# Optimization experiments

Measured on AMD Instinct MI355X. Metric: run time of the kernel, lower is better.

Reference implementation:

```python
import jax, jax.numpy as jnp
import numpy as np

TESS = 5  # number of cells
N_POINTS = 16_777_216


def _make_basis(nc):
    # Continuity constraints of piecewise-affine velocity v(x)=a_c x + b_c at
    # interior knots x_i = i/nc:  a_i x_i + b_i - a_{i+1} x_i - b_{i+1} = 0.
    L = np.zeros((nc - 1, 2 * nc), dtype=np.float64)
    for i in range(1, nc):
        xb = i / nc
        L[i - 1, 2 * (i - 1)] = xb
        L[i - 1, 2 * (i - 1) + 1] = 1.0
        L[i - 1, 2 * i] = -xb
        L[i - 1, 2 * i + 1] = -1.0
    _, _, Vt = np.linalg.svd(L)
    B = Vt[nc - 1:].T  # (2*nc, nc+1) orthonormal null-space basis ('svd')
    return B.astype(np.float32)


def setup_inputs() -> dict:
    key = jax.random.key(0)
    k1, k2 = jax.random.split(key)
    x = jax.random.uniform(k1, (N_POINTS,), dtype=jnp.float32)
    theta = jax.random.normal(k2, (1, TESS + 1), dtype=jnp.float32) * 0.5
    B = jnp.asarray(_make_basis(TESS))
    return {"x": x, "theta": theta, "B": B}


def reference(x, theta, B):
    EPS = 1e-7
    TINY = 1e-12
    BIG = 1e10
    nc = B.shape[0] // 2
    x = jnp.clip(x, EPS, 1.0 - EPS)
    A = (B @ theta[0]).reshape(nc, 2)  # per-cell affine velocity [a_c, b_c]
    a_all, b_all = A[:, 0], A[:, 1]
    c0 = jnp.clip(jnp.floor(x * nc), 0, nc - 1).astype(jnp.int32)

    def step(carry, _):
        xc, c, t, logder = carry
        a = a_all[c]
        b = b_all[c]
        v = a * xc + b
        big = jnp.abs(a) > 1e-8
        sa = jnp.where(big, a, 1.0)
        eat = jnp.exp(a * t)
        # exact in-cell ODE solution psi(x, t)
        psi = jnp.where(big, xc * eat + (b / sa) * (eat - 1.0), xc + b * t)
        right = v >= 0
        xb = jnp.where(right, (c + 1).astype(xc.dtype), c.astype(xc.dtype)) / nc
        den = xc + b / sa
        sden = jnp.where(jnp.abs(den) > TINY, den, TINY)
        ratio = (xb + b / sa) / sden
        thit_a = jnp.log(jnp.maximum(ratio, TINY)) / sa  # time to reach boundary
        sb = jnp.where(jnp.abs(b) > TINY, b, TINY)
        thit_b = (xb - xc) / sb
        thit = jnp.where(big, thit_a, thit_b)
        valid = (jnp.abs(v) > TINY) & (thit >= 0.0) & jnp.where(big, ratio > 0.0, True)
        thit = jnp.where(valid, thit, BIG)
        hits = thit < t
        dt = jnp.where(hits, thit, t)
        x_new = jnp.where(hits, xb, psi)
        c_new = jnp.where(hits, jnp.clip(c + jnp.where(right, 1, -1), 0, nc - 1), c)
        return (x_new, c_new, t - dt, logder + a * dt), None

    init = (x, c0, jnp.ones_like(x), jnp.zeros_like(x))
    (z, _, _, logder), _ = jax.lax.scan(step, init, None, length=nc + 2)
    # log(dz/dx) = sum_c a_c * dt_c  (derivative of flow is exp of integrated slope)
    return z, logder
```

## Files before the change

kernel.cpp:

```cpp
#include <hip/hip_runtime.h>

#define NC 5
#define VEC 8

typedef float fvec4 __attribute__((ext_vector_type(4)));

__global__ __launch_bounds__(256) void flow_cpab_kernel(
    const float* __restrict__ x, const float* __restrict__ theta,
    const float* __restrict__ B, float* __restrict__ out, int n)
{
    __shared__ float4 s_k0[NC];
    __shared__ float4 s_q[12];
    __shared__ float4 s_thr[12];
    __shared__ float4 s_pA[60];
    __shared__ float4 s_pB[60];

    const int tid = threadIdx.x;
    const float EPS  = 1e-7f;
    const float TINY = 1e-12f;
    const float BIG  = 1e10f;
    const float LOG_TINY = -27.631021115928547f;

    const int base = (blockIdx.x * blockDim.x + tid) * VEC;
    float xs[VEC];
    const bool inb  = (base < n);
    const bool full = inb && (base + VEC <= n);
    if (full) {
        float4 x0 = *(const float4*)(x + base);
        float4 x1 = *(const float4*)(x + base + 4);
        xs[0]=x0.x; xs[1]=x0.y; xs[2]=x0.z; xs[3]=x0.w;
        xs[4]=x1.x; xs[5]=x1.y; xs[6]=x1.z; xs[7]=x1.w;
    } else {
        for (int p = 0; p < VEC; ++p)
            xs[p] = (inb && base + p < n) ? x[base + p] : 0.5f;
    }

    if (tid < 12) {
        float a[NC], b[NC], bosa[NC], isa[NC], isb[NC];
        #pragma unroll
        for (int c = 0; c < NC; ++c) {
            float av = 0.f, bv = 0.f;
            #pragma unroll
            for (int j = 0; j < 6; ++j) {
                float th = theta[j];
                av = fmaf(B[(2 * c) * 6 + j], th, av);
                bv = fmaf(B[(2 * c + 1) * 6 + j], th, bv);
            }
            const bool  big = fabsf(av) > 1e-8f;
            const float sa  = big ? av : 1.0f;
            const float sb  = (fabsf(bv) > TINY) ? bv : TINY;
            a[c] = av; b[c] = bv;
            bosa[c] = bv / sa; isa[c] = 1.0f / sa; isb[c] = 1.0f / sb;
        }
        if (tid < NC)
            s_k0[tid] = make_float4(a[tid], b[tid], bosa[tid], isa[tid]);

        const int d  = tid / 6;
        const int jb = tid % 6;

        {
            const int  c0 = (d == 0) ? jb - 1 : jb;
            const int  cs = (c0 >= 0 && c0 < NC) ? c0 : 0;
            const float xb  = (float)jb / 5.0f;
            const float num = xb + bosa[cs];
            const float Lb  = __logf(fmaxf(fabsf(num), 1e-30f));
            const float sgn = (num >= 0.f) ? 1.f : -1.f;
            s_q[tid] = make_float4(Lb, sgn, xb, isb[cs]);
        }

        float Ccum = 0.f, Lcum = 0.f;
        float th[4] = {BIG, BIG, BIG, BIG};
        for (int m = 0; m < 5; ++m) {
            const int  cf   = (d == 0) ? (jb + m) : (jb - 1 - m);
            const bool sent = (cf < 0) || (cf >= NC);
            const float xe  = (d == 0) ? ((float)cf / 5.0f)
                                       : ((float)(cf + 1) / 5.0f);
            const float af    = sent ? 0.f : a[cf];
            const float bf    = sent ? 0.f : b[cf];
            const float bosaf = sent ? 0.f : bosa[cf];
            s_pA[tid * 5 + m] = make_float4(Ccum, Lcum, xe, af);
            s_pB[tid * 5 + m] = make_float4(bf, bosaf, 0.f, 0.f);

            float T = BIG;
            if (!sent) {
                const float xL  = (float)cf / 5.0f;
                const float xR  = (float)(cf + 1) / 5.0f;
                const float xce = (d == 0) ? xL : xR;
                const float xbt = (d == 0) ? xR : xL;
                const float v   = fmaf(af, xce, bf);
                const bool  big = fabsf(af) > 1e-8f;
                const float den  = xce + bosaf;
                const float sden = (fabsf(den) > TINY) ? den : TINY;
                const float ratio = __fdividef(xbt + bosaf, sden);
                const float ta = __logf(fmaxf(ratio, TINY)) * isa[cf];
                const float tb = (xbt - xce) * isb[cf];
                float thit = big ? ta : tb;
                const bool valid = (fabsf(v) > TINY) && (thit >= 0.f) &&
                                   (!big || (ratio > 0.f));
                T = valid ? thit : BIG;
            }
            const float newC = Ccum + T;
            if (m < 4) th[m] = newC;
            if (T < BIG) Lcum = fmaf(af, T, Lcum);
            Ccum = newC;
        }
        s_thr[tid] = make_float4(th[0], th[1], th[2], th[3]);
    }
    __syncthreads();

    if (!inb) return;

    float zz[VEC], ll[VEC];
    #pragma unroll
    for (int p = 0; p < VEC; ++p) {
        const float xc = fminf(fmaxf(xs[p], EPS), 1.0f - EPS);
        const int c0 = min((int)(xc * (float)NC), NC - 1);

        const float4 k0 = s_k0[c0];
        const float a = k0.x, b = k0.y, bosa = k0.z, isa = k0.w;
        const bool  big = fabsf(a) > 1e-8f;

        const float v     = fmaf(a, xc, b);
        const bool  right = (v >= 0.0f);
        const int   tix   = (right ? 0 : 6) + c0 + (right ? 1 : 0);
        const float4 q    = s_q[tix];

        const float den  = xc + bosa;
        const float l    = __logf(fmaxf(fabsf(den), TINY));
        const float diff = fmaxf(q.x - l, LOG_TINY);
        const float th_a = diff * isa;
        const float th_b = (q.z - xc) * q.w;
        float thit0 = big ? th_a : th_b;
        const bool valid = (fabsf(v) > TINY) && (thit0 >= 0.0f) &&
                           (!big || (den * q.y > 0.0f));
        thit0 = valid ? thit0 : BIG;

        const bool  hit0 = (thit0 < 1.0f);
        const float tr   = 1.0f - thit0;

        const float4 th = s_thr[tix];
        const int m = (th.x < tr) + (th.y < tr) + (th.z < tr) + (th.w < tr);
        const int pix = tix * 5 + m;
        const float4 pA = s_pA[pix];
        const float4 pB = s_pB[pix];

        const float xe    = hit0 ? pA.z : xc;
        const float t_f   = hit0 ? (tr - pA.x) : 1.0f;
        const float af    = hit0 ? pA.w : a;
        const float bf    = hit0 ? pB.x : b;
        const float bosaf = hit0 ? pB.y : bosa;
        const float lbase = hit0 ? fmaf(a, thit0, pA.y) : 0.0f;

        const bool  bigf = fabsf(af) > 1e-8f;
        const float eat  = __expf(af * t_f);
        zz[p] = bigf ? fmaf(xe, eat, bosaf * (eat - 1.0f))
                     : fmaf(bf, t_f, xe);
        ll[p] = fmaf(af, t_f, lbase);
    }

    if (full) {
        fvec4 z0 = {zz[0], zz[1], zz[2], zz[3]};
        fvec4 z1 = {zz[4], zz[5], zz[6], zz[7]};
        fvec4 l0 = {ll[0], ll[1], ll[2], ll[3]};
        fvec4 l1 = {ll[4], ll[5], ll[6], ll[7]};
        __builtin_nontemporal_store(z0, (fvec4*)(out + base));
        __builtin_nontemporal_store(z1, (fvec4*)(out + base + 4));
        __builtin_nontemporal_store(l0, (fvec4*)(out + n + base));
        __builtin_nontemporal_store(l1, (fvec4*)(out + n + base + 4));
    } else {
        for (int p = 0; p < VEC; ++p) {
            if (base + p < n) {
                out[base + p]     = zz[p];
                out[n + base + p] = ll[p];
            }
        }
    }
}

extern "C" void kernel_launch(void* const* d_in, const int* in_sizes, int n_in,
                              void* d_out, int out_size, void* d_ws, size_t ws_size,
                              hipStream_t stream) {
    const float* x     = (const float*)d_in[0];
    const float* theta = (const float*)d_in[1];
    const float* B     = (const float*)d_in[2];
    float* out = (float*)d_out;
    const int n = in_sizes[0];

    const int threads = 256;
    const int per_block = threads * VEC;
    const int blocks = (n + per_block - 1) / per_block;
    flow_cpab_kernel<<<blocks, threads, 0, stream>>>(x, theta, B, out, n);
}
```

Measured before the change: 194.7 us.

## Precompute flow tables in a separate setup kernel and shrink per-thread vector width

Moves the per-block computation of the affine coefficients and boundary-crossing tables into a one-block setup kernel that writes them to workspace. The main kernel copies a packed table into shared memory and keeps a/b in registers, selected by cell index. It also halves the points per thread from 8 to 4 and repacks the lookup tables to use fewer shared-memory loads. The aim is to stop every block from redoing the table math serially before its barrier and to raise occupancy. The cost is an extra kernel launch and a global-memory read of the table by every block.

```diff
diff --git a/kernel.cpp b/kernel.cpp
--- a/kernel.cpp
+++ b/kernel.cpp
@@ -1,90 +1,70 @@
 #include <hip/hip_runtime.h>
 
 #define NC 5
-#define VEC 8
+#define VEC 4
 
 typedef float fvec4 __attribute__((ext_vector_type(4)));
 
-__global__ __launch_bounds__(256) void flow_cpab_kernel(
-    const float* __restrict__ x, const float* __restrict__ theta,
-    const float* __restrict__ B, float* __restrict__ out, int n)
+
+__global__ void setup_kernel(const float* __restrict__ theta,
+                             const float* __restrict__ B,
+                             float* __restrict__ ws)
 {
-    __shared__ float4 s_k0[NC];
-    __shared__ float4 s_q[12];
-    __shared__ float4 s_thr[12];
-    __shared__ float4 s_pA[60];
-    __shared__ float4 s_pB[60];
-
     const int tid = threadIdx.x;
-    const float EPS  = 1e-7f;
-    const float TINY = 1e-12f;
-    const float BIG  = 1e10f;
-    const float LOG_TINY = -27.631021115928547f;
-
-    const int base = (blockIdx.x * blockDim.x + tid) * VEC;
-    float xs[VEC];
-    const bool inb  = (base < n);
-    const bool full = inb && (base + VEC <= n);
-    if (full) {
-        float4 x0 = *(const float4*)(x + base);
-        float4 x1 = *(const float4*)(x + base + 4);
-        xs[0]=x0.x; xs[1]=x0.y; xs[2]=x0.z; xs[3]=x0.w;
-        xs[4]=x1.x; xs[5]=x1.y; xs[6]=x1.z; xs[7]=x1.w;
-    } else {
-        for (int p = 0; p < VEC; ++p)
-            xs[p] = (inb && base + p < n) ? x[base + p] : 0.5f;
-    }
+    const float TINY = 1e-12f, BIG = 1e10f;
+
+    float a[NC], b[NC], bosa[NC], isa[NC], isb[NC];
+    #pragma unroll
+    for (int c = 0; c < NC; ++c) {
+        float av = 0.f, bv = 0.f;
+        #pragma unroll
+        for (int j = 0; j < 6; ++j) {
+            float th = theta[j];
+            av = fmaf(B[(2 * c) * 6 + j], th, av);
+            bv = fmaf(B[(2 * c + 1) * 6 + j], th, bv);
+        }
+        const bool  big = fabsf(av) > 1e-8f;
+        const float sa  = big ? av : 1.0f;
+        const float sb  = (fabsf(bv) > TINY) ? bv : TINY;
+        a[c] = av; b[c] = bv;
+        bosa[c] = bv / sa; isa[c] = 1.0f / sa; isb[c] = 1.0f / sb;
+    }
+
+    if (tid < 10) ws[336 + tid] = (tid < 5) ? a[tid] : b[tid - 5];
 
     if (tid < 12) {
-        float a[NC], b[NC], bosa[NC], isa[NC], isb[NC];
-        #pragma unroll
-        for (int c = 0; c < NC; ++c) {
-            float av = 0.f, bv = 0.f;
-            #pragma unroll
-            for (int j = 0; j < 6; ++j) {
-                float th = theta[j];
-                av = fmaf(B[(2 * c) * 6 + j], th, av);
-                bv = fmaf(B[(2 * c + 1) * 6 + j], th, bv);
-            }
-            const bool  big = fabsf(av) > 1e-8f;
-            const float sa  = big ? av : 1.0f;
-            const float sb  = (fabsf(bv) > TINY) ? bv : TINY;
-            a[c] = av; b[c] = bv;
-            bosa[c] = bv / sa; isa[c] = 1.0f / sa; isb[c] = 1.0f / sb;
-        }
-        if (tid < NC)
-            s_k0[tid] = make_float4(a[tid], b[tid], bosa[tid], isa[tid]);
-
         const int d  = tid / 6;
         const int jb = tid % 6;
-
-        {
-            const int  c0 = (d == 0) ? jb - 1 : jb;
-            const int  cs = (c0 >= 0 && c0 < NC) ? c0 : 0;
-            const float xb  = (float)jb / 5.0f;
-            const float num = xb + bosa[cs];
-            const float Lb  = __logf(fmaxf(fabsf(num), 1e-30f));
-            const float sgn = (num >= 0.f) ? 1.f : -1.f;
-            s_q[tid] = make_float4(Lb, sgn, xb, isb[cs]);
-        }
+        const int c0r = (d == 0) ? jb - 1 : jb;
+        const int cs  = min(max(c0r, 0), NC - 1);
+        const float xb  = (float)jb * 0.2f;
+        const float num = xb + bosa[cs];
+        const float Lb  = __logf(fmaxf(fabsf(num), 1e-30f));
+        ws[tid * 4 + 0] = bosa[cs];
+        ws[tid * 4 + 1] = isa[cs];
+        ws[tid * 4 + 2] = Lb;
+        ws[tid * 4 + 3] = num;
 
         float Ccum = 0.f, Lcum = 0.f;
         float th[4] = {BIG, BIG, BIG, BIG};
         for (int m = 0; m < 5; ++m) {
             const int  cf   = (d == 0) ? (jb + m) : (jb - 1 - m);
             const bool sent = (cf < 0) || (cf >= NC);
-            const float xe  = (d == 0) ? ((float)cf / 5.0f)
-                                       : ((float)(cf + 1) / 5.0f);
+            const float xe  = (d == 0) ? (float)cf * 0.2f
+                                       : (float)(cf + 1) * 0.2f;
             const float af    = sent ? 0.f : a[cf];
-            const float bf    = sent ? 0.f : b[cf];
             const float bosaf = sent ? 0.f : bosa[cf];
-            s_pA[tid * 5 + m] = make_float4(Ccum, Lcum, xe, af);
-            s_pB[tid * 5 + m] = make_float4(bf, bosaf, 0.f, 0.f);
+            const int pix = tid * 5 + m;
+            ws[96 + pix * 4 + 0] = af;
+            ws[96 + pix * 4 + 1] = bosaf;
+            ws[96 + pix * 4 + 2] = xe;
+            ws[96 + pix * 4 + 3] = Lcum;
 
             float T = BIG;
             if (!sent) {
-                const float xL  = (float)cf / 5.0f;
-                const float xR  = (float)(cf + 1) / 5.0f;
+                const float bf  = b[cf];
+                const float xL  = (float)cf * 0.2f;
+                const float xR  = (float)(cf + 1) * 0.2f;
                 const float xce = (d == 0) ? xL : xR;
                 const float xbt = (d == 0) ? xR : xL;
                 const float v   = fmaf(af, xce, bf);
@@ -99,13 +79,46 @@
                                    (!big || (ratio > 0.f));
                 T = valid ? thit : BIG;
             }
-            const float newC = Ccum + T;
-            if (m < 4) th[m] = newC;
+            if (m < 4) th[m] = Ccum + T;
             if (T < BIG) Lcum = fmaf(af, T, Lcum);
-            Ccum = newC;
+            Ccum += T;
         }
-        s_thr[tid] = make_float4(th[0], th[1], th[2], th[3]);
-    }
+        ws[48 + tid * 4 + 0] = th[0];
+        ws[48 + tid * 4 + 1] = th[1];
+        ws[48 + tid * 4 + 2] = th[2];
+        ws[48 + tid * 4 + 3] = th[3];
+    }
+}
+
+__global__ __launch_bounds__(256) void flow_cpab_kernel(
+    const float* __restrict__ x, const float* __restrict__ ws,
+    float* __restrict__ out, int n)
+{
+    __shared__ float4 s[84];
+
+    const int tid = threadIdx.x;
+    const float EPS  = 1e-7f;
+    const float TINY = 1e-12f;
+    const float BIG  = 1e10f;
+    const float LOG_TINY = -27.631021115928547f;
+
+    const int base = (blockIdx.x * blockDim.x + tid) * VEC;
+    float xs[VEC];
+    const bool inb  = (base < n);
+    const bool full = inb && (base + VEC <= n);
+    if (full) {
+        float4 xv = *(const float4*)(x + base);
+        xs[0] = xv.x; xs[1] = xv.y; xs[2] = xv.z; xs[3] = xv.w;
+    } else {
+        for (int p = 0; p < VEC; ++p)
+            xs[p] = (inb && base + p < n) ? x[base + p] : 0.5f;
+    }
+
+    if (tid < 84) s[tid] = ((const float4*)ws)[tid];
+
+    const float a0 = ws[336], a1 = ws[337], a2 = ws[338], a3 = ws[339], a4 = ws[340];
+    const float b0 = ws[341], b1 = ws[342], b2 = ws[343], b3 = ws[344], b4 = ws[345];
+
     __syncthreads();
 
     if (!inb) return;
@@ -116,42 +129,48 @@
         const float xc = fminf(fmaxf(xs[p], EPS), 1.0f - EPS);
         const int c0 = min((int)(xc * (float)NC), NC - 1);
 
-        const float4 k0 = s_k0[c0];
-        const float a = k0.x, b = k0.y, bosa = k0.z, isa = k0.w;
-        const bool  big = fabsf(a) > 1e-8f;
+        const float a = (c0 == 0) ? a0 : (c0 == 1) ? a1 : (c0 == 2) ? a2
+                       : (c0 == 3) ? a3 : a4;
+        const float b = (c0 == 0) ? b0 : (c0 == 1) ? b1 : (c0 == 2) ? b2
+                       : (c0 == 3) ? b3 : b4;
 
         const float v     = fmaf(a, xc, b);
         const bool  right = (v >= 0.0f);
-        const int   tix   = (right ? 0 : 6) + c0 + (right ? 1 : 0);
-        const float4 q    = s_q[tix];
-
-        const float den  = xc + bosa;
+        const int   jb    = right ? (c0 + 1) : c0;
+        const int   tix   = (right ? 0 : 6) + jb;
+
+        const float4 r1 = s[tix];
+        const float4 th = s[12 + tix];
+
+        const float xb   = 0.2f * (float)jb;
+        const float den  = xc + r1.x;
         const float l    = __logf(fmaxf(fabsf(den), TINY));
-        const float diff = fmaxf(q.x - l, LOG_TINY);
-        const float th_a = diff * isa;
-        const float th_b = (q.z - xc) * q.w;
+        const float diff = fmaxf(r1.z - l, LOG_TINY);
+        const bool  big  = fabsf(a) > 1e-8f;
+        const float th_a = diff * r1.y;
+        const float sb   = (fabsf(b) > TINY) ? b : TINY;
+        const float th_b = (xb - xc) * __builtin_amdgcn_rcpf(sb);
         float thit0 = big ? th_a : th_b;
         const bool valid = (fabsf(v) > TINY) && (thit0 >= 0.0f) &&
-                           (!big || (den * q.y > 0.0f));
+                           (!big || (den * r1.w > 0.0f));
         thit0 = valid ? thit0 : BIG;
 
         const bool  hit0 = (thit0 < 1.0f);
         const float tr   = 1.0f - thit0;
 
-        const float4 th = s_thr[tix];
         const int m = (th.x < tr) + (th.y < tr) + (th.z < tr) + (th.w < tr);
-        const int pix = tix * 5 + m;
-        const float4 pA = s_pA[pix];
-        const float4 pB = s_pB[pix];
-
-        const float xe    = hit0 ? pA.z : xc;
-        const float t_f   = hit0 ? (tr - pA.x) : 1.0f;
-        const float af    = hit0 ? pA.w : a;
-        const float bf    = hit0 ? pB.x : b;
-        const float bosaf = hit0 ? pB.y : bosa;
-        const float lbase = hit0 ? fmaf(a, thit0, pA.y) : 0.0f;
+        const float Ccum = (m == 0) ? 0.0f : (m == 1) ? th.x
+                          : (m == 2) ? th.y : (m == 3) ? th.z : th.w;
+        const float4 pk = s[24 + tix * 5 + m];
+
+        const float af    = hit0 ? pk.x : a;
+        const float bosaf = hit0 ? pk.y : r1.x;
+        const float xe    = hit0 ? pk.z : xc;
+        const float lbase = hit0 ? fmaf(a, thit0, pk.w) : 0.0f;
+        const float t_f   = hit0 ? (tr - Ccum) : 1.0f;
 
         const bool  bigf = fabsf(af) > 1e-8f;
+        const float bf   = bigf ? af * bosaf : bosaf;
         const float eat  = __expf(af * t_f);
         zz[p] = bigf ? fmaf(xe, eat, bosaf * (eat - 1.0f))
                      : fmaf(bf, t_f, xe);
@@ -159,14 +178,10 @@
     }
 
     if (full) {
-        fvec4 z0 = {zz[0], zz[1], zz[2], zz[3]};
-        fvec4 z1 = {zz[4], zz[5], zz[6], zz[7]};
-        fvec4 l0 = {ll[0], ll[1], ll[2], ll[3]};
-        fvec4 l1 = {ll[4], ll[5], ll[6], ll[7]};
-        __builtin_nontemporal_store(z0, (fvec4*)(out + base));
-        __builtin_nontemporal_store(z1, (fvec4*)(out + base + 4));
-        __builtin_nontemporal_store(l0, (fvec4*)(out + n + base));
-        __builtin_nontemporal_store(l1, (fvec4*)(out + n + base + 4));
+        fvec4 zv = {zz[0], zz[1], zz[2], zz[3]};
+        fvec4 lv = {ll[0], ll[1], ll[2], ll[3]};
+        __builtin_nontemporal_store(zv, (fvec4*)(out + base));
+        __builtin_nontemporal_store(lv, (fvec4*)(out + n + base));
     } else {
         for (int p = 0; p < VEC; ++p) {
             if (base + p < n) {
@@ -184,10 +199,13 @@
     const float* theta = (const float*)d_in[1];
     const float* B     = (const float*)d_in[2];
     float* out = (float*)d_out;
+    float* ws  = (float*)d_ws;
     const int n = in_sizes[0];
+
+    setup_kernel<<<1, 64, 0, stream>>>(theta, B, ws);
 
     const int threads = 256;
     const int per_block = threads * VEC;
     const int blocks = (n + per_block - 1) / per_block;
-    flow_cpab_kernel<<<blocks, threads, 0, stream>>>(x, theta, B, out, n);
+    flow_cpab_kernel<<<blocks, threads, 0, stream>>>(x, ws, out, n);
 }
```

Result: no change. 191.0 us (-1.9%).
